# Kernel tuning notes

Measured on AMD Instinct MI355X. Metric: run time of the kernel, lower is better.

The kernel has to match this reference:

```python
import jax, jax.numpy as jnp
import numpy as np

N = 100000      # nodes
E = 800000      # edges (avg degree 8)
F = 61          # num_node_features (embedding dim); node feat = F+3 = 64 with pos
D = 64          # hidden_dim
OUT = 32        # output_dim
TYPES = 100     # num_node_types
G = 64          # number of graphs in the batch (global_mean_pool segments)
L = 4           # num_layers per SE3Transformer (from transformer_config)


def _mk(k, shape):
    return jax.random.normal(k, shape, jnp.float32) * 0.1


def setup_inputs() -> dict:
    key = jax.random.key(0)
    ks = jax.random.split(key, 24)
    din = F + 3  # cat([pos, embedding(z)])
    inp = {
        "pos": jax.random.normal(ks[0], (N, 3), jnp.float32),
        "z": jax.random.randint(ks[1], (N,), 0, TYPES),
        "edge_index": jax.random.randint(ks[2], (2, E), 0, N),
        "batch": jnp.sort(jax.random.randint(ks[3], (N,), 0, G)),
        "emb": _mk(ks[4], (TYPES, F)),
        # transformer1: input proj din->D, then L message-passing layers at width D
        "t1_Win": _mk(ks[5], (din, D)),
        "t1_W1": _mk(ks[6], (L, 2 * D + 1, D)), "t1_b1": jnp.zeros((L, D), jnp.float32),
        "t1_W2": _mk(ks[7], (L, D, D)),        "t1_b2": jnp.zeros((L, D), jnp.float32),
        "t1_W3": _mk(ks[8], (L, 2 * D, D)),    "t1_b3": jnp.zeros((L, D), jnp.float32),
        # transformer2: input proj D->D, then L layers at width D
        "t2_Win": _mk(ks[9], (D, D)),
        "t2_W1": _mk(ks[10], (L, 2 * D + 1, D)), "t2_b1": jnp.zeros((L, D), jnp.float32),
        "t2_W2": _mk(ks[11], (L, D, D)),         "t2_b2": jnp.zeros((L, D), jnp.float32),
        "t2_W3": _mk(ks[12], (L, 2 * D, D)),     "t2_b3": jnp.zeros((L, D), jnp.float32),
        # final Linear(hidden_dim, output_dim)
        "Wlin": _mk(ks[13], (D, OUT)), "blin": jnp.zeros((OUT,), jnp.float32),
    }
    return inp


def _transformer(h, pos, src, dst, Win, W1, b1, W2, b2, W3, b3):
    """Equivariant graph transformer block: input projection + L distance-
    conditioned message-passing layers with residual updates."""
    h = h @ Win  # [N, D]
    # squared pairwise distance per edge -> rotation/translation invariant
    d2 = jnp.sum((pos[src] - pos[dst]) ** 2, axis=-1, keepdims=True)  # [E, 1]

    def layer(h, p):
        W1, b1, W2, b2, W3, b3 = p
        m = jnp.concatenate([h[src], h[dst], d2], axis=-1)        # [E, 2D+1]
        m = jax.nn.relu(m @ W1 + b1) @ W2 + b2                    # [E, D]
        agg = jax.ops.segment_sum(m, dst, num_segments=N)          # [N, D]
        h = h + jax.nn.relu(jnp.concatenate([h, agg], axis=-1) @ W3 + b3)
        return h, None

    h, _ = jax.lax.scan(layer, h, (W1, b1, W2, b2, W3, b3))
    return h


def reference(pos, z, edge_index, batch, emb,
              t1_Win, t1_W1, t1_b1, t1_W2, t1_b2, t1_W3, t1_b3,
              t2_Win, t2_W1, t2_b1, t2_W2, t2_b2, t2_W3, t2_b3,
              Wlin, blin):
    src, dst = edge_index[0], edge_index[1]
    x = jnp.concatenate([pos, emb[z]], axis=-1)  # [N, 3+F]
    x = jax.nn.relu(_transformer(x, pos, src, dst, t1_Win, t1_W1, t1_b1, t1_W2, t1_b2, t1_W3, t1_b3))
    x = jax.nn.relu(_transformer(x, pos, src, dst, t2_Win, t2_W1, t2_b1, t2_W2, t2_b2, t2_W3, t2_b3))
    x = x @ Wlin + blin  # [N, OUT]
    # global_mean_pool over graph ids
    counts = jax.ops.segment_sum(jnp.ones((N,), x.dtype), batch, num_segments=G)
    pooled = jax.ops.segment_sum(x, batch, num_segments=G) / jnp.clip(counts, 1.0)[:, None]
    return pooled  # [G, OUT]
```

## Files before the change

kernel.cpp:

```cpp
#include <hip/hip_runtime.h>
#include <hip/hip_bf16.h>

typedef unsigned short u16;
typedef unsigned int   u32;
typedef short bf16x8 __attribute__((ext_vector_type(8)));
typedef float f32x4  __attribute__((ext_vector_type(4)));

#define NN 100000
#define EE 800000
#define NTILE 6250
#define NTB   1563
#define EBLK  1536
#define TOTW  (EBLK * 4)
#define SCB   98
#define GMAX  (NN + EE / 8 + 2)

#define MFMA16(a,b,c) __builtin_amdgcn_mfma_f32_16x16x32_bf16(a,b,c,0,0,0)

__device__ __forceinline__ float b2f(u16 u) {
    u32 x = ((u32)u) << 16;
    return __uint_as_float(x);
}
__device__ __forceinline__ u16 f2b(float f) {
    __hip_bfloat16 h = __float2bfloat16(f);
    return *reinterpret_cast<u16*>(&h);
}
__device__ __forceinline__ void splt(float v, u16& hi, u16& lo) {
    hi = f2b(v);
    lo = f2b(v - b2f(hi));
}

__global__ __launch_bounds__(256) void k_embed(const float* __restrict__ pos,
                                               const int* __restrict__ z,
                                               const float* __restrict__ emb,
                                               u16* __restrict__ xc) {
    int gid = blockIdx.x * 256 + threadIdx.x;
    int i = gid >> 6, f = gid & 63;
    float v = (f < 3) ? pos[i * 3 + f] : emb[(long)z[i] * 61 + (f - 3)];
    u16 hi, lo; splt(v, hi, lo);
    xc[(long)i * 128 + f] = hi;
    xc[(long)i * 128 + 64 + f] = lo;
}

__global__ __launch_bounds__(256) void k_relu_split(const u16* __restrict__ hbx,
                                                    u16* __restrict__ xc) {
    int gid = blockIdx.x * 256 + threadIdx.x;
    int i = gid >> 6, f = gid & 63;
    float v = b2f(hbx[(long)i * 128 + f]) + b2f(hbx[(long)i * 128 + 64 + f]);
    v = fmaxf(v, 0.f);
    u16 hi, lo; splt(v, hi, lo);
    xc[(long)i * 128 + f] = hi;
    xc[(long)i * 128 + 64 + f] = lo;
}

__global__ __launch_bounds__(256) void k_deg(const int* __restrict__ dst,
                                             int* __restrict__ deg) {
    int e = blockIdx.x * 256 + threadIdx.x;
    if (e < EE) atomicAdd(&deg[dst[e]], 1);
}

__global__ __launch_bounds__(1024) void k_scanA(const int* __restrict__ deg,
                                                int* __restrict__ part) {
    __shared__ int s[1024];
    int i = blockIdx.x * 1024 + threadIdx.x;
    int v = (i < NN) ? deg[i] : 0;
    s[threadIdx.x] = v;
    __syncthreads();
    for (int off = 512; off > 0; off >>= 1) {
        if ((int)threadIdx.x < off) s[threadIdx.x] += s[threadIdx.x + off];
        __syncthreads();
    }
    if (threadIdx.x == 0) part[blockIdx.x] = s[0];
}

__global__ void k_scanB(int* __restrict__ part) {
    if (threadIdx.x == 0 && blockIdx.x == 0) {
        int run = 0;
        for (int b = 0; b < SCB; ++b) { int v = part[b]; part[b] = run; run += v; }
        part[SCB] = run;
    }
}

__global__ __launch_bounds__(1024) void k_scanC(const int* __restrict__ deg,
                                                const int* __restrict__ part,
                                                int* __restrict__ rowptr) {
    __shared__ int s[1024];
    int i = blockIdx.x * 1024 + threadIdx.x;
    int v = (i < NN) ? deg[i] : 0;
    s[threadIdx.x] = v;
    __syncthreads();
    for (int off = 1; off < 1024; off <<= 1) {
        int t = ((int)threadIdx.x >= off) ? s[threadIdx.x - off] : 0;
        __syncthreads();
        s[threadIdx.x] += t;
        __syncthreads();
    }
    int incl = s[threadIdx.x];
    if (i < NN) rowptr[i] = part[blockIdx.x] + incl - v;
    if (i == NN - 1) rowptr[NN] = part[SCB];
}

__global__ __launch_bounds__(256) void k_scatter(const int* __restrict__ src,
                                                 const int* __restrict__ dst,
                                                 const float* __restrict__ pos,
                                                 int* __restrict__ cursor,
                                                 int* __restrict__ srcc,
                                                 float* __restrict__ d2c) {
    int e = blockIdx.x * 256 + threadIdx.x;
    if (e >= EE) return;
    if (e < 16) { srcc[EE + e] = 0; d2c[EE + e] = 0.f; }
    int d = dst[e], s = src[e];
    int p = atomicAdd(&cursor[d], 1);
    srcc[p] = s;
    float dx = pos[s * 3 + 0] - pos[d * 3 + 0];
    float dy = pos[s * 3 + 1] - pos[d * 3 + 1];
    float dz = pos[s * 3 + 2] - pos[d * 3 + 2];
    d2c[p] = dx * dx + dy * dy + dz * dz;
}

__global__ __launch_bounds__(256) void k_ngrp(const int* __restrict__ deg,
                                              int* __restrict__ ngrp) {
    int i = blockIdx.x * 256 + threadIdx.x;
    if (i < NN) ngrp[i] = (deg[i] + 7) >> 3;
}

__global__ __launch_bounds__(256) void k_gfill(const int* __restrict__ deg,
                                               const int* __restrict__ rowptr,
                                               const int* __restrict__ grp_ptr,
                                               int* __restrict__ gnode,
                                               int* __restrict__ gstart,
                                               int* __restrict__ gcnt) {
    int n = blockIdx.x * 256 + threadIdx.x;
    if (n >= NN) return;
    int d = deg[n];
    int ng = (d + 7) >> 3;
    int base = grp_ptr[n], rp = rowptr[n];
    for (int k = 0; k < ng; ++k) {
        gnode[base + k] = n;
        gstart[base + k] = rp + 8 * k;
        int cc = d - 8 * k; if (cc > 8) cc = 8;
        gcnt[base + k] = cc;
    }
}

__global__ __launch_bounds__(256) void k_swz(const float* t1W1, const float* t1W2, const float* t1W3,
                                             const float* t2W1, const float* t2W2, const float* t2W3,
                                             const float* t1Win, const float* t2Win,
                                             u16* __restrict__ WsA, u16* __restrict__ WsB) {
    int gid = blockIdx.x * 256 + threadIdx.x;
    if (gid < 163840) {
        int L = gid / 20480;
        int r = gid % 20480;
        const float* W1 = (L < 4 ? t1W1 : t2W1) + (size_t)(L & 3) * 129 * 64;
        const float* W2 = (L < 4 ? t1W2 : t2W2) + (size_t)(L & 3) * 64 * 64;
        const float* W3 = (L < 4 ? t1W3 : t2W3) + (size_t)(L & 3) * 128 * 64;
        float w;
        int rr, f, e, lane, j, row, col;
        if (r < 8192) { rr = r; f = rr >> 9; e = rr & 511; lane = e >> 3; j = e & 7;
            row = (f >> 2) * 32 + (lane >> 4) * 8 + j; col = (f & 3) * 16 + (lane & 15);
            w = W1[row * 64 + col];
        } else if (r < 12288) { rr = r - 8192; f = rr >> 9; e = rr & 511; lane = e >> 3; j = e & 7;
            row = (f >> 2) * 32 + (lane >> 4) * 8 + j; col = (f & 3) * 16 + (lane & 15);
            w = W2[row * 64 + col];
        } else { rr = r - 12288; f = rr >> 9; e = rr & 511; lane = e >> 3; j = e & 7;
            row = (f >> 2) * 32 + (lane >> 4) * 8 + j; col = (f & 3) * 16 + (lane & 15);
            w = W3[row * 64 + col];
        }
        u16 hi, lo; splt(w, hi, lo);
        WsA[(size_t)L * 40960 + r] = hi;
        WsA[(size_t)L * 40960 + 20480 + r] = lo;
    } else {
        int t = gid - 163840;
        int sel = (t < 4096) ? 0 : 1;
        int rr = t & 4095;
        const float* Win = sel ? t2Win : t1Win;
        int f = rr >> 9, e = rr & 511, lane = e >> 3, j = e & 7;
        int row = (f >> 2) * 32 + (lane >> 4) * 8 + j;
        int col = (f & 3) * 16 + (lane & 15);
        float w = Win[row * 64 + col];
        u16 hi, lo; splt(w, hi, lo);
        WsB[sel * 8192 + rr] = hi;
        WsB[sel * 8192 + 4096 + rr] = lo;
    }
}

__global__ __launch_bounds__(256) void k_proj_mfma(const u16* __restrict__ xc,
                                                   const u16* __restrict__ WinS,
                                                   u16* __restrict__ hbx) {
    int tile = blockIdx.x * 4 + (threadIdx.x >> 6);
    if (tile >= NTILE) return;
    int lane = threadIdx.x & 63, c = lane & 15, g = lane >> 4;
    int n0 = tile * 16, nr = n0 + c;
    const bf16x8* Wh = (const bf16x8*)WinS;
    const bf16x8* Wl = (const bf16x8*)(WinS + 4096);
    const bf16x8* p = (const bf16x8*)(xc + (long)nr * 128);
    bf16x8 A0h = p[g], A1h = p[g + 4], A0l = p[g + 8], A1l = p[g + 12];
#pragma unroll
    for (int nt = 0; nt < 4; ++nt) {
        f32x4 acc = {0.f, 0.f, 0.f, 0.f};
        acc = MFMA16(A0h, Wh[nt * 64 + lane], acc);
        acc = MFMA16(A1h, Wh[(4 + nt) * 64 + lane], acc);
        acc = MFMA16(A0l, Wh[nt * 64 + lane], acc);
        acc = MFMA16(A1l, Wh[(4 + nt) * 64 + lane], acc);
        acc = MFMA16(A0h, Wl[nt * 64 + lane], acc);
        acc = MFMA16(A1h, Wl[(4 + nt) * 64 + lane], acc);
#pragma unroll
        for (int r = 0; r < 4; ++r) {
            long n = n0 + 4 * g + r;
            u16 hi, lo; splt(acc[r], hi, lo);
            hbx[n * 128 + nt * 16 + c] = hi;
            hbx[n * 128 + 64 + nt * 16 + c] = lo;
        }
    }
}

__global__ __launch_bounds__(256) void k_dsthalf(const u16* __restrict__ hbx,
                                                 const u16* __restrict__ Wsl,
                                                 const float* __restrict__ b1,
                                                 float* __restrict__ accb) {
    int tile = blockIdx.x * 4 + (threadIdx.x >> 6);
    if (tile >= NTILE) return;
    int lane = threadIdx.x & 63, c = lane & 15, g = lane >> 4;
    int n0 = tile * 16, nr = n0 + c;
    const bf16x8* W1h = (const bf16x8*)Wsl;
    const bf16x8* W1l = (const bf16x8*)(Wsl + 20480);
    const bf16x8* p = (const bf16x8*)(hbx + (long)nr * 128);
    bf16x8 A0h = p[g], A1h = p[g + 4], A0l = p[g + 8], A1l = p[g + 12];
#pragma unroll
    for (int nt = 0; nt < 4; ++nt) {
        float bv = b1[nt * 16 + c];
        f32x4 acc = {bv, bv, bv, bv};
        acc = MFMA16(A0h, W1h[(8 + nt) * 64 + lane], acc);
        acc = MFMA16(A1h, W1h[(12 + nt) * 64 + lane], acc);
        acc = MFMA16(A0l, W1h[(8 + nt) * 64 + lane], acc);
        acc = MFMA16(A1l, W1h[(12 + nt) * 64 + lane], acc);
        acc = MFMA16(A0h, W1l[(8 + nt) * 64 + lane], acc);
        acc = MFMA16(A1h, W1l[(12 + nt) * 64 + lane], acc);
#pragma unroll
        for (int r = 0; r < 4; ++r)
            accb[(long)(n0 + 4 * g + r) * 64 + nt * 16 + c] = acc[r];
    }
}

__global__ __launch_bounds__(256) void k_edges_mfma(const u16* __restrict__ hbx,
                                                    float* __restrict__ sgrp,
                                                    const float* __restrict__ d2c,
                                                    const int* __restrict__ srcc,
                                                    const int* __restrict__ gnode,
                                                    const int* __restrict__ gstart,
                                                    const int* __restrict__ gcnt,
                                                    const int* __restrict__ grp_ptr,
                                                    const u16* __restrict__ Wsl,
                                                    const float* __restrict__ W1f,
                                                    const float* __restrict__ accb) {
    int lane = threadIdx.x & 63;
    int wid = blockIdx.x * 4 + (threadIdx.x >> 6);
    int c = lane & 15, g = lane >> 4;
    const bf16x8* W1H = (const bf16x8*)Wsl;
    const bf16x8* W1L = (const bf16x8*)(Wsl + 20480);
    bf16x8 w1h[2][4], w1l[2][4];
#pragma unroll
    for (int ks = 0; ks < 2; ++ks)
#pragma unroll
        for (int nt = 0; nt < 4; ++nt) {
            w1h[ks][nt] = W1H[(ks * 4 + nt) * 64 + lane];
            w1l[ks][nt] = W1L[(ks * 4 + nt) * 64 + lane];
        }
    float wdc[4];
#pragma unroll
    for (int nt = 0; nt < 4; ++nt) wdc[nt] = W1f[128 * 64 + nt * 16 + c];

    int G = grp_ptr[NN];
    int T = (G + 1) >> 1;

    for (int ti = wid; ti < T; ti += TOTW) {
        int ga = 2 * ti, gb = 2 * ti + 1;
        int na = gnode[ga], sa = gstart[ga], ca = gcnt[ga];
        int nb = na, sb = sa, cb = 0;
        if (gb < G) { nb = gnode[gb]; sb = gstart[gb]; cb = gcnt[gb]; }

        int nsel = (g < 2) ? na : nb;
        int ssel = (g < 2) ? sa : sb;
        int csel = (g < 2) ? ca : cb;
        int ro = 4 * (g & 1);

        float base[4];
#pragma unroll
        for (int nt = 0; nt < 4; ++nt)
            base[nt] = accb[(long)nsel * 64 + nt * 16 + c];

        int t = (c < 8) ? (sa + c) : (sb + c - 8);
        int s = srcc[t];
        const bf16x8* sp = (const bf16x8*)(hbx + (long)s * 128);
        bf16x8 A0h = sp[g], A1h = sp[g + 4], A0l = sp[g + 8], A1l = sp[g + 12];

        float dq[4];
#pragma unroll
        for (int r = 0; r < 4; ++r) dq[r] = d2c[ssel + ro + r];

        f32x4 sv4;
        float sv[4];
#pragma unroll
        for (int nt = 0; nt < 4; ++nt) {
            f32x4 ci;
#pragma unroll
            for (int r = 0; r < 4; ++r) ci[r] = base[nt] + dq[r] * wdc[nt];
            ci = MFMA16(A0h, w1h[0][nt], ci);
            ci = MFMA16(A1h, w1h[1][nt], ci);
            ci = MFMA16(A0l, w1h[0][nt], ci);
            ci = MFMA16(A1l, w1h[1][nt], ci);
            ci = MFMA16(A0h, w1l[0][nt], ci);
            ci = MFMA16(A1h, w1l[1][nt], ci);
            float s4 = 0.f;
#pragma unroll
            for (int r = 0; r < 4; ++r)
                s4 += (ro + r < csel) ? fmaxf(ci[r], 0.f) : 0.f;
            s4 += __shfl_xor(s4, 16);
            sv[nt] = s4;
        }
        (void)sv4;
        if (g == 0) {
#pragma unroll
            for (int nt = 0; nt < 4; ++nt)
                sgrp[(long)ga * 64 + nt * 16 + c] = sv[nt];
        }
        if (g == 2 && gb < G) {
#pragma unroll
            for (int nt = 0; nt < 4; ++nt)
                sgrp[(long)gb * 64 + nt * 16 + c] = sv[nt];
        }
    }
}

__global__ __launch_bounds__(256) void k_node2(u16* __restrict__ hbx,
                                               const float* __restrict__ sgrp,
                                               const int* __restrict__ grp_ptr,
                                               const int* __restrict__ deg,
                                               const u16* __restrict__ Wsl,
                                               const float* __restrict__ b2,
                                               const float* __restrict__ b3,
                                               const u16* __restrict__ WslN,
                                               const float* __restrict__ b1N,
                                               float* __restrict__ accb) {
    __shared__ u16 th[4][16 * 72];
    __shared__ u16 tl[4][16 * 72];
    int w = threadIdx.x >> 6, lane = threadIdx.x & 63;
    int tile = blockIdx.x * 4 + w;
    if (tile >= NTILE) return;
    int c = lane & 15, g = lane >> 4;
    int n0 = tile * 16, nr = n0 + c;
    u16* lh = th[w];
    u16* ll = tl[w];

    const bf16x8* W2H = (const bf16x8*)(Wsl + 8192);
    const bf16x8* W2L = (const bf16x8*)(Wsl + 28672);
    const bf16x8* W3H = (const bf16x8*)(Wsl + 12288);
    const bf16x8* W3L = (const bf16x8*)(Wsl + 32768);

    int gp0 = grp_ptr[nr], gp1 = grp_ptr[nr + 1];
    f32x4 sA0 = {0, 0, 0, 0}, sA1 = {0, 0, 0, 0};
    f32x4 sB0 = {0, 0, 0, 0}, sB1 = {0, 0, 0, 0};
    for (int gi = gp0; gi < gp1; ++gi) {
        const f32x4* q = (const f32x4*)(sgrp + (long)gi * 64 + 8 * g);
        const f32x4* q2 = (const f32x4*)(sgrp + (long)gi * 64 + 32 + 8 * g);
        sA0 += q[0]; sA1 += q[1];
        sB0 += q2[0]; sB1 += q2[1];
    }
    bf16x8 S0h, S0l, S1h, S1l;
#pragma unroll
    for (int j = 0; j < 4; ++j) {
        u16 hi, lo;
        splt(sA0[j], hi, lo); S0h[j] = (short)hi; S0l[j] = (short)lo;
        splt(sA1[j], hi, lo); S0h[4 + j] = (short)hi; S0l[4 + j] = (short)lo;
        splt(sB0[j], hi, lo); S1h[j] = (short)hi; S1l[j] = (short)lo;
        splt(sB1[j], hi, lo); S1h[4 + j] = (short)hi; S1l[4 + j] = (short)lo;
    }

    const bf16x8* hp = (const bf16x8*)(hbx + (long)nr * 128);
    bf16x8 H0h = hp[g], H1h = hp[g + 4], H0l = hp[g + 8], H1l = hp[g + 12];

    float dg[4];
#pragma unroll
    for (int r = 0; r < 4; ++r) dg[r] = (float)deg[n0 + 4 * g + r];

#pragma unroll
    for (int nt = 0; nt < 4; ++nt) {
        float b2c = b2[nt * 16 + c];
        f32x4 a = {dg[0] * b2c, dg[1] * b2c, dg[2] * b2c, dg[3] * b2c};
        a = MFMA16(S0h, W2H[nt * 64 + lane], a);
        a = MFMA16(S1h, W2H[(4 + nt) * 64 + lane], a);
        a = MFMA16(S0l, W2H[nt * 64 + lane], a);
        a = MFMA16(S1l, W2H[(4 + nt) * 64 + lane], a);
        a = MFMA16(S0h, W2L[nt * 64 + lane], a);
        a = MFMA16(S1h, W2L[(4 + nt) * 64 + lane], a);
#pragma unroll
        for (int r = 0; r < 4; ++r) {
            u16 hi, lo; splt(a[r], hi, lo);
            lh[(4 * g + r) * 72 + nt * 16 + c] = hi;
            ll[(4 * g + r) * 72 + nt * 16 + c] = lo;
        }
    }
    bf16x8 G0h = *(const bf16x8*)(lh + c * 72 + g * 8);
    bf16x8 G1h = *(const bf16x8*)(lh + c * 72 + 32 + g * 8);
    bf16x8 G0l = *(const bf16x8*)(ll + c * 72 + g * 8);
    bf16x8 G1l = *(const bf16x8*)(ll + c * 72 + 32 + g * 8);

    f32x4 u4[4];
#pragma unroll
    for (int nt = 0; nt < 4; ++nt) {
        float bv = b3[nt * 16 + c];
        f32x4 u = {bv, bv, bv, bv};
        u = MFMA16(H0h, W3H[nt * 64 + lane], u);
        u = MFMA16(H1h, W3H[(4 + nt) * 64 + lane], u);
        u = MFMA16(G0h, W3H[(8 + nt) * 64 + lane], u);
        u = MFMA16(G1h, W3H[(12 + nt) * 64 + lane], u);
        u = MFMA16(H0l, W3H[nt * 64 + lane], u);
        u = MFMA16(H1l, W3H[(4 + nt) * 64 + lane], u);
        u = MFMA16(G0l, W3H[(8 + nt) * 64 + lane], u);
        u = MFMA16(G1l, W3H[(12 + nt) * 64 + lane], u);
        u = MFMA16(H0h, W3L[nt * 64 + lane], u);
        u = MFMA16(H1h, W3L[(4 + nt) * 64 + lane], u);
        u = MFMA16(G0h, W3L[(8 + nt) * 64 + lane], u);
        u = MFMA16(G1h, W3L[(12 + nt) * 64 + lane], u);
        u4[nt] = u;
    }

#pragma unroll
    for (int nt = 0; nt < 4; ++nt)
#pragma unroll
        for (int r = 0; r < 4; ++r) {
            long n = n0 + 4 * g + r;
            long ix = n * 128 + nt * 16 + c;
            float ho = b2f(hbx[ix]) + b2f(hbx[ix + 64]);
            float hn = ho + fmaxf(u4[nt][r], 0.f);
            u16 hi, lo; splt(hn, hi, lo);
            hbx[ix] = hi;
            hbx[ix + 64] = lo;
            lh[(4 * g + r) * 72 + nt * 16 + c] = hi;
            ll[(4 * g + r) * 72 + nt * 16 + c] = lo;
        }

    if (WslN) {
        bf16x8 N0h = *(const bf16x8*)(lh + c * 72 + g * 8);
        bf16x8 N1h = *(const bf16x8*)(lh + c * 72 + 32 + g * 8);
        bf16x8 N0l = *(const bf16x8*)(ll + c * 72 + g * 8);
        bf16x8 N1l = *(const bf16x8*)(ll + c * 72 + 32 + g * 8);
        const bf16x8* W1h = (const bf16x8*)WslN;
        const bf16x8* W1l = (const bf16x8*)(WslN + 20480);
#pragma unroll
        for (int nt = 0; nt < 4; ++nt) {
            float bv = b1N[nt * 16 + c];
            f32x4 a = {bv, bv, bv, bv};
            a = MFMA16(N0h, W1h[(8 + nt) * 64 + lane], a);
            a = MFMA16(N1h, W1h[(12 + nt) * 64 + lane], a);
            a = MFMA16(N0l, W1h[(8 + nt) * 64 + lane], a);
            a = MFMA16(N1l, W1h[(12 + nt) * 64 + lane], a);
            a = MFMA16(N0h, W1l[(8 + nt) * 64 + lane], a);
            a = MFMA16(N1h, W1l[(12 + nt) * 64 + lane], a);
#pragma unroll
            for (int r = 0; r < 4; ++r)
                accb[(long)(n0 + 4 * g + r) * 64 + nt * 16 + c] = a[r];
        }
    }
}

__global__ void k_granges(const int* __restrict__ batch, int* __restrict__ gpt) {
    int g = blockIdx.x * blockDim.x + threadIdx.x;
    if (g > 64) return;
    int lo = 0, hi = NN;
    while (lo < hi) {
        int mid = (lo + hi) >> 1;
        if (batch[mid] < g) lo = mid + 1; else hi = mid;
    }
    gpt[g] = lo;
}

__global__ __launch_bounds__(256) void k_sumrelu(const u16* __restrict__ hbx,
                                                 const int* __restrict__ gpt,
                                                 float* __restrict__ sumh) {
    int g = blockIdx.x >> 3, sp = blockIdx.x & 7;
    int lo = gpt[g], hi = gpt[g + 1];
    int n = hi - lo;
    int per = (n + 7) / 8;
    int s0 = lo + sp * per;
    int s1 = s0 + per; if (s1 > hi) s1 = hi;
    int lane = threadIdx.x & 63, wv = threadIdx.x >> 6;
    float acc = 0.f;
    for (int i = s0 + wv; i < s1; i += 4) {
        float v = b2f(hbx[(long)i * 128 + lane]) + b2f(hbx[(long)i * 128 + 64 + lane]);
        acc += fmaxf(v, 0.f);
    }
    if (acc != 0.f || wv == 0)
        atomicAdd(&sumh[g * 64 + lane], acc);
}

__global__ __launch_bounds__(256) void k_outgemm(const float* __restrict__ sumh,
                                                 const int* __restrict__ gpt,
                                                 const float* __restrict__ Wlin,
                                                 const float* __restrict__ blin,
                                                 float* __restrict__ out) {
    int idx = blockIdx.x * 256 + threadIdx.x;
    if (idx >= 64 * 32) return;
    int g = idx >> 5, o = idx & 31;
    int cnt = gpt[g + 1] - gpt[g];
    float acc = 0.f;
#pragma unroll 8
    for (int k = 0; k < 64; ++k)
        acc += sumh[g * 64 + k] * Wlin[k * 32 + o];
    out[idx] = (cnt > 0) ? (acc / (float)cnt + blin[o]) : 0.f;
}

extern "C" void kernel_launch(void* const* d_in, const int* in_sizes, int n_in,
                              void* d_out, int out_size, void* d_ws, size_t ws_size,
                              hipStream_t stream) {
    const float* pos    = (const float*)d_in[0];
    const int*   z      = (const int*)d_in[1];
    const int*   ei     = (const int*)d_in[2];
    const int*   batch  = (const int*)d_in[3];
    const float* emb    = (const float*)d_in[4];
    const float* t1_Win = (const float*)d_in[5];
    const float* t1_W1  = (const float*)d_in[6];
    const float* t1_b1  = (const float*)d_in[7];
    const float* t1_W2  = (const float*)d_in[8];
    const float* t1_b2  = (const float*)d_in[9];
    const float* t1_W3  = (const float*)d_in[10];
    const float* t1_b3  = (const float*)d_in[11];
    const float* t2_Win = (const float*)d_in[12];
    const float* t2_W1  = (const float*)d_in[13];
    const float* t2_b1  = (const float*)d_in[14];
    const float* t2_W2  = (const float*)d_in[15];
    const float* t2_b2  = (const float*)d_in[16];
    const float* t2_W3  = (const float*)d_in[17];
    const float* t2_b3  = (const float*)d_in[18];
    const float* Wlin   = (const float*)d_in[19];
    const float* blin   = (const float*)d_in[20];

    const int* srcI = ei;
    const int* dstI = ei + EE;

    char* ws = (char*)d_ws;
    size_t off = 0;
    auto alloc = [&](size_t bytes) -> void* {
        void* p = ws + off;
        off += (bytes + 255) / 256 * 256;
        return p;
    };
    float* accb    = (float*)alloc((size_t)NN * 64 * 4);
    u16*   hbx     = (u16*)alloc((size_t)NN * 128 * 2);
    float* sgrp    = (float*)alloc((size_t)GMAX * 64 * 4);
    int*   rowptr  = (int*)alloc((size_t)(NN + 1) * 4);
    int*   deg     = (int*)alloc((size_t)NN * 4);
    int*   cursor  = (int*)alloc((size_t)NN * 4);
    int*   ngrpA   = (int*)alloc((size_t)NN * 4);
    int*   grp_ptr = (int*)alloc((size_t)(NN + 1) * 4);
    int*   gnode   = (int*)alloc((size_t)GMAX * 4);
    int*   gstart  = (int*)alloc((size_t)GMAX * 4);
    int*   gcnt    = (int*)alloc((size_t)GMAX * 4);
    int*   srcc    = (int*)alloc((size_t)(EE + 16) * 4);
    float* d2c     = (float*)alloc((size_t)(EE + 16) * 4);
    int*   gpt     = (int*)alloc(65 * 4);
    float* sumh    = (float*)alloc(64 * 64 * 4);
    int*   part    = (int*)alloc((SCB + 1) * 4);
    u16*   WsA     = (u16*)alloc((size_t)8 * 40960 * 2);
    u16*   WsB     = (u16*)alloc((size_t)16384 * 2);

    u16* xc = (u16*)accb;

    k_embed<<<NN * 64 / 256, 256, 0, stream>>>(pos, z, emb, xc);
    hipMemsetAsync(deg, 0, (size_t)NN * 4, stream);
    k_deg<<<(EE + 255) / 256, 256, 0, stream>>>(dstI, deg);
    k_scanA<<<SCB, 1024, 0, stream>>>(deg, part);
    k_scanB<<<1, 64, 0, stream>>>(part);
    k_scanC<<<SCB, 1024, 0, stream>>>(deg, part, rowptr);
    hipMemcpyAsync(cursor, rowptr, (size_t)NN * 4, hipMemcpyDeviceToDevice, stream);
    k_scatter<<<(EE + 255) / 256, 256, 0, stream>>>(srcI, dstI, pos, cursor, srcc, d2c);
    k_ngrp<<<(NN + 255) / 256, 256, 0, stream>>>(deg, ngrpA);
    k_scanA<<<SCB, 1024, 0, stream>>>(ngrpA, part);
    k_scanB<<<1, 64, 0, stream>>>(part);
    k_scanC<<<SCB, 1024, 0, stream>>>(ngrpA, part, grp_ptr);
    k_gfill<<<(NN + 255) / 256, 256, 0, stream>>>(deg, rowptr, grp_ptr, gnode, gstart, gcnt);
    k_swz<<<172032 / 256, 256, 0, stream>>>(t1_W1, t1_W2, t1_W3, t2_W1, t2_W2, t2_W3,
                                            t1_Win, t2_Win, WsA, WsB);
    k_granges<<<1, 128, 0, stream>>>(batch, gpt);

    k_proj_mfma<<<NTB, 256, 0, stream>>>(xc, WsB, hbx);
    k_dsthalf<<<NTB, 256, 0, stream>>>(hbx, WsA, t1_b1, accb);
    for (int l = 0; l < 4; ++l) {
        const u16* Wsl = WsA + (size_t)l * 40960;
        k_edges_mfma<<<EBLK, 256, 0, stream>>>(hbx, sgrp, d2c, srcc, gnode, gstart,
                                               gcnt, grp_ptr, Wsl,
                                               t1_W1 + (size_t)l * 129 * 64, accb);
        const u16* WslN = (l < 3) ? (WsA + (size_t)(l + 1) * 40960) : nullptr;
        const float* b1N = (l < 3) ? (t1_b1 + (size_t)(l + 1) * 64) : nullptr;
        k_node2<<<NTB, 256, 0, stream>>>(hbx, sgrp, grp_ptr, deg, Wsl,
                                         t1_b2 + (size_t)l * 64, t1_b3 + (size_t)l * 64,
                                         WslN, b1N, accb);
    }

    k_relu_split<<<NN * 64 / 256, 256, 0, stream>>>(hbx, xc);
    k_proj_mfma<<<NTB, 256, 0, stream>>>(xc, WsB + 8192, hbx);
    k_dsthalf<<<NTB, 256, 0, stream>>>(hbx, WsA + (size_t)4 * 40960, t2_b1, accb);
    for (int l = 0; l < 4; ++l) {
        const u16* Wsl = WsA + (size_t)(4 + l) * 40960;
        k_edges_mfma<<<EBLK, 256, 0, stream>>>(hbx, sgrp, d2c, srcc, gnode, gstart,
                                               gcnt, grp_ptr, Wsl,
                                               t2_W1 + (size_t)l * 129 * 64, accb);
        const u16* WslN = (l < 3) ? (WsA + (size_t)(5 + l) * 40960) : nullptr;
        const float* b1N = (l < 3) ? (t2_b1 + (size_t)(l + 1) * 64) : nullptr;
        k_node2<<<NTB, 256, 0, stream>>>(hbx, sgrp, grp_ptr, deg, Wsl,
                                         t2_b2 + (size_t)l * 64, t2_b3 + (size_t)l * 64,
                                         WslN, b1N, accb);
    }

    hipMemsetAsync(sumh, 0, 64 * 64 * 4, stream);
    k_sumrelu<<<64 * 8, 256, 0, stream>>>(hbx, gpt, sumh);
    k_outgemm<<<8, 256, 0, stream>>>(sumh, gpt, Wlin, blin, (float*)d_out);
}
```

Measured before the change: 1.061 ms.

## Fuse embedding and relu-split into projections, transpose per-node bias buffer layout

The embedding gather and the relu/hi-lo split kernels are folded into the two input-projection kernels, which now build their bf16 hi/lo operands in registers. This removes two elementwise launches and their round-trip through global memory. The per-node W1 dst-half buffer is stored in a column-interleaved layout, so each lane writes and reads one 16-byte vector instead of four strided scalars. The edge kernel grid also grows from 1536 to 1792 blocks.

```diff
diff --git a/kernel.cpp b/kernel.cpp
--- a/kernel.cpp
+++ b/kernel.cpp
@@ -10,7 +10,7 @@
 #define EE 800000
 #define NTILE 6250
 #define NTB   1563
-#define EBLK  1536
+#define EBLK  1792
 #define TOTW  (EBLK * 4)
 #define SCB   98
 #define GMAX  (NN + EE / 8 + 2)
@@ -28,29 +28,6 @@
 __device__ __forceinline__ void splt(float v, u16& hi, u16& lo) {
     hi = f2b(v);
     lo = f2b(v - b2f(hi));
-}
-
-__global__ __launch_bounds__(256) void k_embed(const float* __restrict__ pos,
-                                               const int* __restrict__ z,
-                                               const float* __restrict__ emb,
-                                               u16* __restrict__ xc) {
-    int gid = blockIdx.x * 256 + threadIdx.x;
-    int i = gid >> 6, f = gid & 63;
-    float v = (f < 3) ? pos[i * 3 + f] : emb[(long)z[i] * 61 + (f - 3)];
-    u16 hi, lo; splt(v, hi, lo);
-    xc[(long)i * 128 + f] = hi;
-    xc[(long)i * 128 + 64 + f] = lo;
-}
-
-__global__ __launch_bounds__(256) void k_relu_split(const u16* __restrict__ hbx,
-                                                    u16* __restrict__ xc) {
-    int gid = blockIdx.x * 256 + threadIdx.x;
-    int i = gid >> 6, f = gid & 63;
-    float v = b2f(hbx[(long)i * 128 + f]) + b2f(hbx[(long)i * 128 + 64 + f]);
-    v = fmaxf(v, 0.f);
-    u16 hi, lo; splt(v, hi, lo);
-    xc[(long)i * 128 + f] = hi;
-    xc[(long)i * 128 + 64 + f] = lo;
 }
 
 __global__ __launch_bounds__(256) void k_deg(const int* __restrict__ dst,
@@ -184,17 +161,29 @@
     }
 }
 
-__global__ __launch_bounds__(256) void k_proj_mfma(const u16* __restrict__ xc,
-                                                   const u16* __restrict__ WinS,
-                                                   u16* __restrict__ hbx) {
+__global__ __launch_bounds__(256) void k_proj1(const float* __restrict__ pos,
+                                               const int* __restrict__ z,
+                                               const float* __restrict__ emb,
+                                               const u16* __restrict__ WinS,
+                                               u16* __restrict__ hbx) {
     int tile = blockIdx.x * 4 + (threadIdx.x >> 6);
     if (tile >= NTILE) return;
     int lane = threadIdx.x & 63, c = lane & 15, g = lane >> 4;
     int n0 = tile * 16, nr = n0 + c;
+    int zr = z[nr];
+    const float* er = emb + (long)zr * 61 - 3;
+    bf16x8 A0h, A0l, A1h, A1l;
+#pragma unroll
+    for (int j = 0; j < 8; ++j) {
+        int f = 8 * g + j;
+        float v1 = (f < 3) ? pos[nr * 3 + (f < 3 ? f : 0)] : er[f];
+        float v2 = er[32 + 8 * g + j];
+        u16 hi, lo;
+        splt(v1, hi, lo); A0h[j] = (short)hi; A0l[j] = (short)lo;
+        splt(v2, hi, lo); A1h[j] = (short)hi; A1l[j] = (short)lo;
+    }
     const bf16x8* Wh = (const bf16x8*)WinS;
     const bf16x8* Wl = (const bf16x8*)(WinS + 4096);
-    const bf16x8* p = (const bf16x8*)(xc + (long)nr * 128);
-    bf16x8 A0h = p[g], A1h = p[g + 4], A0l = p[g + 8], A1l = p[g + 12];
 #pragma unroll
     for (int nt = 0; nt < 4; ++nt) {
         f32x4 acc = {0.f, 0.f, 0.f, 0.f};
@@ -214,10 +203,48 @@
     }
 }
 
+__global__ __launch_bounds__(256) void k_proj2(const u16* __restrict__ WinS,
+                                               u16* __restrict__ hbx) {
+    int tile = blockIdx.x * 4 + (threadIdx.x >> 6);
+    if (tile >= NTILE) return;
+    int lane = threadIdx.x & 63, c = lane & 15, g = lane >> 4;
+    int n0 = tile * 16, nr = n0 + c;
+    const bf16x8* p = (const bf16x8*)(hbx + (long)nr * 128);
+    bf16x8 h0 = p[g], h1 = p[g + 4], l0 = p[g + 8], l1 = p[g + 12];
+    bf16x8 A0h, A0l, A1h, A1l;
+#pragma unroll
+    for (int j = 0; j < 8; ++j) {
+        float v1 = fmaxf(b2f((u16)h0[j]) + b2f((u16)l0[j]), 0.f);
+        float v2 = fmaxf(b2f((u16)h1[j]) + b2f((u16)l1[j]), 0.f);
+        u16 hi, lo;
+        splt(v1, hi, lo); A0h[j] = (short)hi; A0l[j] = (short)lo;
+        splt(v2, hi, lo); A1h[j] = (short)hi; A1l[j] = (short)lo;
+    }
+    const bf16x8* Wh = (const bf16x8*)WinS;
+    const bf16x8* Wl = (const bf16x8*)(WinS + 4096);
+#pragma unroll
+    for (int nt = 0; nt < 4; ++nt) {
+        f32x4 acc = {0.f, 0.f, 0.f, 0.f};
+        acc = MFMA16(A0h, Wh[nt * 64 + lane], acc);
+        acc = MFMA16(A1h, Wh[(4 + nt) * 64 + lane], acc);
+        acc = MFMA16(A0l, Wh[nt * 64 + lane], acc);
+        acc = MFMA16(A1l, Wh[(4 + nt) * 64 + lane], acc);
+        acc = MFMA16(A0h, Wl[nt * 64 + lane], acc);
+        acc = MFMA16(A1h, Wl[(4 + nt) * 64 + lane], acc);
+#pragma unroll
+        for (int r = 0; r < 4; ++r) {
+            long n = n0 + 4 * g + r;
+            u16 hi, lo; splt(acc[r], hi, lo);
+            hbx[n * 128 + nt * 16 + c] = hi;
+            hbx[n * 128 + 64 + nt * 16 + c] = lo;
+        }
+    }
+}
+
 __global__ __launch_bounds__(256) void k_dsthalf(const u16* __restrict__ hbx,
                                                  const u16* __restrict__ Wsl,
                                                  const float* __restrict__ b1,
-                                                 float* __restrict__ accb) {
+                                                 float* __restrict__ accbT) {
     int tile = blockIdx.x * 4 + (threadIdx.x >> 6);
     if (tile >= NTILE) return;
     int lane = threadIdx.x & 63, c = lane & 15, g = lane >> 4;
@@ -226,6 +253,7 @@
     const bf16x8* W1l = (const bf16x8*)(Wsl + 20480);
     const bf16x8* p = (const bf16x8*)(hbx + (long)nr * 128);
     bf16x8 A0h = p[g], A1h = p[g + 4], A0l = p[g + 8], A1l = p[g + 12];
+    f32x4 acc4[4];
 #pragma unroll
     for (int nt = 0; nt < 4; ++nt) {
         float bv = b1[nt * 16 + c];
@@ -236,9 +264,12 @@
         acc = MFMA16(A1l, W1h[(12 + nt) * 64 + lane], acc);
         acc = MFMA16(A0h, W1l[(8 + nt) * 64 + lane], acc);
         acc = MFMA16(A1h, W1l[(12 + nt) * 64 + lane], acc);
-#pragma unroll
-        for (int r = 0; r < 4; ++r)
-            accb[(long)(n0 + 4 * g + r) * 64 + nt * 16 + c] = acc[r];
+        acc4[nt] = acc;
+    }
+#pragma unroll
+    for (int r = 0; r < 4; ++r) {
+        f32x4 w = {acc4[0][r], acc4[1][r], acc4[2][r], acc4[3][r]};
+        *(f32x4*)(accbT + (long)(n0 + 4 * g + r) * 64 + c * 4) = w;
     }
 }
 
@@ -252,7 +283,7 @@
                                                     const int* __restrict__ grp_ptr,
                                                     const u16* __restrict__ Wsl,
                                                     const float* __restrict__ W1f,
-                                                    const float* __restrict__ accb) {
+                                                    const float* __restrict__ accbT) {
     int lane = threadIdx.x & 63;
     int wid = blockIdx.x * 4 + (threadIdx.x >> 6);
     int c = lane & 15, g = lane >> 4;
@@ -284,10 +315,7 @@
         int csel = (g < 2) ? ca : cb;
         int ro = 4 * (g & 1);
 
-        float base[4];
-#pragma unroll
-        for (int nt = 0; nt < 4; ++nt)
-            base[nt] = accb[(long)nsel * 64 + nt * 16 + c];
+        f32x4 bse = *(const f32x4*)(accbT + (long)nsel * 64 + c * 4);
 
         int t = (c < 8) ? (sa + c) : (sb + c - 8);
         int s = srcc[t];
@@ -298,13 +326,12 @@
 #pragma unroll
         for (int r = 0; r < 4; ++r) dq[r] = d2c[ssel + ro + r];
 
-        f32x4 sv4;
         float sv[4];
 #pragma unroll
         for (int nt = 0; nt < 4; ++nt) {
             f32x4 ci;
 #pragma unroll
-            for (int r = 0; r < 4; ++r) ci[r] = base[nt] + dq[r] * wdc[nt];
+            for (int r = 0; r < 4; ++r) ci[r] = bse[nt] + dq[r] * wdc[nt];
             ci = MFMA16(A0h, w1h[0][nt], ci);
             ci = MFMA16(A1h, w1h[1][nt], ci);
             ci = MFMA16(A0l, w1h[0][nt], ci);
@@ -318,7 +345,6 @@
             s4 += __shfl_xor(s4, 16);
             sv[nt] = s4;
         }
-        (void)sv4;
         if (g == 0) {
 #pragma unroll
             for (int nt = 0; nt < 4; ++nt)
@@ -341,7 +367,7 @@
                                                const float* __restrict__ b3,
                                                const u16* __restrict__ WslN,
                                                const float* __restrict__ b1N,
-                                               float* __restrict__ accb) {
+                                               float* __restrict__ accbT) {
     __shared__ u16 th[4][16 * 72];
     __shared__ u16 tl[4][16 * 72];
     int w = threadIdx.x >> 6, lane = threadIdx.x & 63;
@@ -447,6 +473,7 @@
         bf16x8 N1l = *(const bf16x8*)(ll + c * 72 + 32 + g * 8);
         const bf16x8* W1h = (const bf16x8*)WslN;
         const bf16x8* W1l = (const bf16x8*)(WslN + 20480);
+        f32x4 acc4[4];
 #pragma unroll
         for (int nt = 0; nt < 4; ++nt) {
             float bv = b1N[nt * 16 + c];
@@ -457,9 +484,12 @@
             a = MFMA16(N1l, W1h[(12 + nt) * 64 + lane], a);
             a = MFMA16(N0h, W1l[(8 + nt) * 64 + lane], a);
             a = MFMA16(N1h, W1l[(12 + nt) * 64 + lane], a);
-#pragma unroll
-            for (int r = 0; r < 4; ++r)
-                accb[(long)(n0 + 4 * g + r) * 64 + nt * 16 + c] = a[r];
+            acc4[nt] = a;
+        }
+#pragma unroll
+        for (int r = 0; r < 4; ++r) {
+            f32x4 wv = {acc4[0][r], acc4[1][r], acc4[2][r], acc4[3][r]};
+            *(f32x4*)(accbT + (long)(n0 + 4 * g + r) * 64 + c * 4) = wv;
         }
     }
 }
@@ -545,7 +575,7 @@
         off += (bytes + 255) / 256 * 256;
         return p;
     };
-    float* accb    = (float*)alloc((size_t)NN * 64 * 4);
+    float* accbT   = (float*)alloc((size_t)NN * 64 * 4);
     u16*   hbx     = (u16*)alloc((size_t)NN * 128 * 2);
     float* sgrp    = (float*)alloc((size_t)GMAX * 64 * 4);
     int*   rowptr  = (int*)alloc((size_t)(NN + 1) * 4);
@@ -564,9 +594,6 @@
     u16*   WsA     = (u16*)alloc((size_t)8 * 40960 * 2);
     u16*   WsB     = (u16*)alloc((size_t)16384 * 2);
 
-    u16* xc = (u16*)accb;
-
-    k_embed<<<NN * 64 / 256, 256, 0, stream>>>(pos, z, emb, xc);
     hipMemsetAsync(deg, 0, (size_t)NN * 4, stream);
     k_deg<<<(EE + 255) / 256, 256, 0, stream>>>(dstI, deg);
     k_scanA<<<SCB, 1024, 0, stream>>>(deg, part);
@@ -583,33 +610,32 @@
                                             t1_Win, t2_Win, WsA, WsB);
     k_granges<<<1, 128, 0, stream>>>(batch, gpt);
 
-    k_proj_mfma<<<NTB, 256, 0, stream>>>(xc, WsB, hbx);
-    k_dsthalf<<<NTB, 256, 0, stream>>>(hbx, WsA, t1_b1, accb);
+    k_proj1<<<NTB, 256, 0, stream>>>(pos, z, emb, WsB, hbx);
+    k_dsthalf<<<NTB, 256, 0, stream>>>(hbx, WsA, t1_b1, accbT);
     for (int l = 0; l < 4; ++l) {
         const u16* Wsl = WsA + (size_t)l * 40960;
         k_edges_mfma<<<EBLK, 256, 0, stream>>>(hbx, sgrp, d2c, srcc, gnode, gstart,
                                                gcnt, grp_ptr, Wsl,
-                                               t1_W1 + (size_t)l * 129 * 64, accb);
+                                               t1_W1 + (size_t)l * 129 * 64, accbT);
         const u16* WslN = (l < 3) ? (WsA + (size_t)(l + 1) * 40960) : nullptr;
         const float* b1N = (l < 3) ? (t1_b1 + (size_t)(l + 1) * 64) : nullptr;
         k_node2<<<NTB, 256, 0, stream>>>(hbx, sgrp, grp_ptr, deg, Wsl,
                                          t1_b2 + (size_t)l * 64, t1_b3 + (size_t)l * 64,
-                                         WslN, b1N, accb);
-    }
-
-    k_relu_split<<<NN * 64 / 256, 256, 0, stream>>>(hbx, xc);
-    k_proj_mfma<<<NTB, 256, 0, stream>>>(xc, WsB + 8192, hbx);
-    k_dsthalf<<<NTB, 256, 0, stream>>>(hbx, WsA + (size_t)4 * 40960, t2_b1, accb);
+                                         WslN, b1N, accbT);
+    }
+
+    k_proj2<<<NTB, 256, 0, stream>>>(WsB + 8192, hbx);
+    k_dsthalf<<<NTB, 256, 0, stream>>>(hbx, WsA + (size_t)4 * 40960, t2_b1, accbT);
     for (int l = 0; l < 4; ++l) {
         const u16* Wsl = WsA + (size_t)(4 + l) * 40960;
         k_edges_mfma<<<EBLK, 256, 0, stream>>>(hbx, sgrp, d2c, srcc, gnode, gstart,
                                                gcnt, grp_ptr, Wsl,
-                                               t2_W1 + (size_t)l * 129 * 64, accb);
+                                               t2_W1 + (size_t)l * 129 * 64, accbT);
         const u16* WslN = (l < 3) ? (WsA + (size_t)(5 + l) * 40960) : nullptr;
         const float* b1N = (l < 3) ? (t2_b1 + (size_t)(l + 1) * 64) : nullptr;
         k_node2<<<NTB, 256, 0, stream>>>(hbx, sgrp, grp_ptr, deg, Wsl,
                                          t2_b2 + (size_t)l * 64, t2_b3 + (size_t)l * 64,
-                                         WslN, b1N, accb);
+                                         WslN, b1N, accbT);
     }
 
     hipMemsetAsync(sumh, 0, 64 * 64 * 4, stream);
```

New measurement: 1.057 ms. Within noise of the previous version (-0.3%).
